# Kernel optimization log

Hardware: AMD Instinct MI355X
Metric: run time of the kernel (lower is better)

The kernel has to match this reference:

```python
import jax, jax.numpy as jnp
import numpy as np

B, NQ, NKV, D, H, HD = 8, 1024, 2048, 1024, 16, 64  # inner_dim = H*HD = 1024


def setup_inputs() -> dict:
    key = jax.random.key(0)
    ks = jax.random.split(key, 10)
    s = 0.02
    return {
        "latent": jax.random.normal(ks[0], (B, NQ, D), jnp.float32),
        "data": jax.random.normal(ks[1], (B, NKV, D), jnp.float32),
        "wq": jax.random.normal(ks[2], (D, H * HD), jnp.float32) * s,
        "bq": jax.random.normal(ks[3], (H * HD,), jnp.float32) * s,
        "wk": jax.random.normal(ks[4], (D, H * HD), jnp.float32) * s,
        "bk": jax.random.normal(ks[5], (H * HD,), jnp.float32) * s,
        "wv": jax.random.normal(ks[6], (D, H * HD), jnp.float32) * s,
        "bv": jax.random.normal(ks[7], (H * HD,), jnp.float32) * s,
        "wo": jax.random.normal(ks[8], (H * HD, D), jnp.float32) * s,
        "bo": jax.random.normal(ks[9], (D,), jnp.float32) * s,
    }


def reference(latent, data, wq, bq, wk, bk, wv, bv, wo, bo):
    scale = HD ** -0.5
    # projections: [b, n, H*HD] -> [b, h, n, d]
    def split_heads(t):
        b, n, _ = t.shape
        return t.reshape(b, n, H, HD).transpose(0, 2, 1, 3)

    q = split_heads(latent @ wq + bq)   # [b, h, nq, d]
    k = split_heads(data @ wk + bk)     # [b, h, nkv, d]
    v = split_heads(data @ wv + bv)     # [b, h, nkv, d]

    scores = jnp.einsum("bhid,bhjd->bhij", q, k) * scale  # [b, h, nq, nkv]
    att = jax.nn.softmax(scores, axis=-1)                  # dropout p=0 (eval)
    out = jnp.einsum("bhij,bhjd->bhid", att, v)            # [b, h, nq, d]
    out = out.transpose(0, 2, 1, 3).reshape(B, NQ, H * HD)
    return out @ wo + bo
```

## Files before the change

### kernel.cpp

```cpp
#include <hip/hip_runtime.h>
#include <hip/hip_bf16.h>
#include <math.h>


using short8  = __attribute__((ext_vector_type(8))) short;
using f32x4   = __attribute__((ext_vector_type(4))) float;
using uint4v  = __attribute__((ext_vector_type(4))) unsigned int;

__device__ __forceinline__ ushort f2bf(float f) {
    unsigned u = __builtin_bit_cast(unsigned, f);
    u = (u + 0x7FFFu + ((u >> 16) & 1u)) >> 16;
    return (ushort)u;
}
__device__ __forceinline__ unsigned pack_bf2(float lo, float hi) {
    unsigned ulo = __builtin_bit_cast(unsigned, lo) + 0x8000u;
    unsigned uhi = __builtin_bit_cast(unsigned, hi) + 0x8000u;
    return __builtin_amdgcn_perm(uhi, ulo, 0x07060302);
}

__device__ __forceinline__ void gld_lds16(const ushort* g, ushort* l) {
    __builtin_amdgcn_global_load_lds(
        (const __attribute__((address_space(1))) unsigned int*)(const void*)g,
        (__attribute__((address_space(3))) unsigned int*)(void*)l,
        16, 0, 0);
}

__global__ void prep_fused(const float* __restrict__ latent, const float* __restrict__ data,
                           const float* __restrict__ wq, const float* __restrict__ wk,
                           const float* __restrict__ wv, const float* __restrict__ wo,
                           ushort* __restrict__ latB, ushort* __restrict__ datB,
                           ushort* __restrict__ wqT, ushort* __restrict__ wkT,
                           ushort* __restrict__ wvT, ushort* __restrict__ woT) {
    __shared__ ushort tile[32][33];
    const int bx  = blockIdx.x;
    const int tid = threadIdx.x;
    if (bx < 12288) {
        const float* in = (bx < 4096) ? latent : data;
        ushort* out     = (bx < 4096) ? latB : datB;
        int idx = (bx < 4096) ? bx : bx - 4096;
        int i = (idx * 256 + tid) * 8;
        float4 a = *(const float4*)(in + i);
        float4 b = *(const float4*)(in + i + 4);
        short8 o;
        o[0] = (short)f2bf(a.x); o[1] = (short)f2bf(a.y);
        o[2] = (short)f2bf(a.z); o[3] = (short)f2bf(a.w);
        o[4] = (short)f2bf(b.x); o[5] = (short)f2bf(b.y);
        o[6] = (short)f2bf(b.z); o[7] = (short)f2bf(b.w);
        *(short8*)(out + i) = o;
        return;
    }
    int rem = bx - 12288;
    int z   = rem >> 10;
    int bxx = rem & 31;
    int byy = (rem >> 5) & 31;
    const float* in = (z == 0) ? wq : (z == 1) ? wk : (z == 2) ? wv : wo;
    ushort* out     = (z == 0) ? wqT : (z == 1) ? wkT : (z == 2) ? wvT : woT;
    int tx = tid & 31, ty = tid >> 5;
    int x = bxx * 32 + tx;
    int y = byy * 32;
#pragma unroll
    for (int i = 0; i < 32; i += 8)
        tile[ty + i][tx] = f2bf(in[(size_t)(y + ty + i) * 1024 + x]);
    __syncthreads();
    int x2 = byy * 32 + tx;
    int y2 = bxx * 32;
#pragma unroll
    for (int i = 0; i < 32; i += 8)
        out[(size_t)(y2 + ty + i) * 1024 + x2] = tile[tx][ty + i];
}

template <int S>
__device__ __forceinline__ void stage_half(const ushort* __restrict__ G, int rbase,
                                           ushort* tile, int H, int kcol,
                                           int wave, int lane) {
#pragma unroll
    for (int c = 0; c < 2; ++c) {
        int rho = c * 64 + wave * 8;
        int gr0 = (rho / S) * (2 * S) + H * S + (rho % S);
        int rig = lane >> 3;
        int q   = (lane & 7) ^ rig;
        gld_lds16(G + (size_t)(rbase + gr0 + rig) * 1024 + kcol + q * 8,
                  tile + gr0 * 64);
    }
}

__device__ __forceinline__ void gemm256_body(
        const ushort* __restrict__ A, const ushort* __restrict__ Bt,
        const float* __restrict__ bias, void* __restrict__ Cv,
        float scale, int mode, int bm, int bn) {
    __shared__ __align__(16) ushort sm[65536];
    ushort* As0 = sm;
    ushort* Bs0 = sm + 16384;
    ushort* As1 = sm + 32768;
    ushort* Bs1 = sm + 49152;

    const int tid  = threadIdx.x;
    const int wave = tid >> 6, lane = tid & 63;
    const int l15 = lane & 15, quad = lane >> 4;
    const int wm = wave >> 2, wn = wave & 3;
    const int m0 = bm * 256, n0 = bn * 256;

    const int rA  = wm * 128 + l15;
    const int rB  = wn * 64 + l15;
    const int cq0 = quad ^ (l15 & 7);
    const int cq1 = (4 + quad) ^ (l15 & 7);

    stage_half<64>(A,  m0, As0, 0, 0,  wave, lane);
    stage_half<32>(Bt, n0, Bs0, 0, 0,  wave, lane);
    stage_half<32>(Bt, n0, Bs0, 1, 0,  wave, lane);
    stage_half<64>(A,  m0, As0, 1, 0,  wave, lane);
    stage_half<64>(A,  m0, As1, 0, 64, wave, lane);
    stage_half<32>(Bt, n0, Bs1, 1, 64, wave, lane);
    stage_half<64>(A,  m0, As1, 1, 64, wave, lane);
    asm volatile("s_waitcnt vmcnt(6)" ::: "memory");
    __builtin_amdgcn_s_barrier();

    f32x4 acc[8][4] = {};

#define LDA(MH)                                                                   \
    _Pragma("unroll")                                                             \
    for (int mi = 0; mi < 4; ++mi) {                                              \
        a[mi][0] = *(const short8*)(Ac + (rA + (MH) * 64 + mi * 16) * 64 + cq0 * 8); \
        a[mi][1] = *(const short8*)(Ac + (rA + (MH) * 64 + mi * 16) * 64 + cq1 * 8); \
    }
#define LDB_ALL                                                                   \
    _Pragma("unroll")                                                             \
    for (int nj = 0; nj < 4; ++nj) {                                              \
        b[nj][0] = *(const short8*)(Bc + (rB + nj * 16) * 64 + cq0 * 8);          \
        b[nj][1] = *(const short8*)(Bc + (rB + nj * 16) * 64 + cq1 * 8);          \
    }
#define MFMA_PHASE(MB, NB)                                                        \
    __builtin_amdgcn_s_barrier();                                                 \
    asm volatile("s_waitcnt lgkmcnt(0)" ::: "memory");                            \
    __builtin_amdgcn_sched_barrier(0);                                            \
    __builtin_amdgcn_s_setprio(1);                                                \
    _Pragma("unroll")                                                             \
    for (int mi = 0; mi < 4; ++mi)                                                \
        _Pragma("unroll")                                                         \
        for (int ni = 0; ni < 2; ++ni)                                            \
            _Pragma("unroll")                                                     \
            for (int kk = 0; kk < 2; ++kk)                                        \
                acc[(MB) * 4 + mi][(NB) * 2 + ni] =                               \
                    __builtin_amdgcn_mfma_f32_16x16x32_bf16(                      \
                        a[mi][kk], b[(NB) * 2 + ni][kk],                          \
                        acc[(MB) * 4 + mi][(NB) * 2 + ni], 0, 0, 0);              \
    __builtin_amdgcn_s_setprio(0);                                                \
    __builtin_amdgcn_s_barrier();

#pragma unroll 2
    for (int g = 0; g < 16; ++g) {
        ushort* Ac = (g & 1) ? As1 : As0;
        ushort* Bc = (g & 1) ? Bs1 : Bs0;
        ushort* Bn = (g & 1) ? Bs0 : Bs1;
        const int k1 = ((g + 1) & 15) * 64;
        const int k2 = ((g + 2) & 15) * 64;
        short8 a[4][2], b[4][2];

        LDA(0) LDB_ALL
        stage_half<32>(Bt, n0, Bn, 0, k1, wave, lane);
        MFMA_PHASE(0, 0)

        stage_half<64>(A, m0, Ac, 0, k2, wave, lane);
        MFMA_PHASE(0, 1)

        LDA(1)
        stage_half<32>(Bt, n0, Bc, 1, k2, wave, lane);
        MFMA_PHASE(1, 1)

        stage_half<64>(A, m0, Ac, 1, k2, wave, lane);
        asm volatile("s_waitcnt vmcnt(6)" ::: "memory");
        MFMA_PHASE(1, 0)
    }
#undef LDA
#undef LDB_ALL
#undef MFMA_PHASE

    asm volatile("s_waitcnt vmcnt(0)" ::: "memory");

    float bvv[4];
    int   cols[4];
#pragma unroll
    for (int n4 = 0; n4 < 4; ++n4) {
        cols[n4] = n0 + wn * 64 + n4 * 16 + l15;
        bvv[n4]  = bias[cols[n4]];
    }
#pragma unroll
    for (int m8 = 0; m8 < 8; ++m8) {
        int rbase = m0 + wm * 128 + m8 * 16 + quad * 4;
#pragma unroll
        for (int n4 = 0; n4 < 4; ++n4) {
            float v[4];
#pragma unroll
            for (int rr = 0; rr < 4; ++rr)
                v[rr] = (acc[m8][n4][rr] + bvv[n4]) * scale;
            if (mode == 1) {
                int kvl = rbase & 2047;
                int pos = (kvl & ~31) + ((kvl >> 2) & 3) * 8 + ((kvl >> 4) & 1) * 4;
                size_t base = ((size_t)((rbase >> 11) * 1024 + cols[n4])) * 2048 + pos;
                uint2 o;
                o.x = pack_bf2(v[0], v[1]);
                o.y = pack_bf2(v[2], v[3]);
                *(uint2*)((ushort*)Cv + base) = o;
            } else if (mode == 0) {
#pragma unroll
                for (int rr = 0; rr < 4; ++rr)
                    ((ushort*)Cv)[(size_t)(rbase + rr) * 1024 + cols[n4]] = f2bf(v[rr]);
            } else {
#pragma unroll
                for (int rr = 0; rr < 4; ++rr)
                    ((float*)Cv)[(size_t)(rbase + rr) * 1024 + cols[n4]] = v[rr];
            }
        }
    }
}

__global__ __launch_bounds__(512, 2) void proj_qkv(
        const ushort* __restrict__ latB, const ushort* __restrict__ datB,
        const ushort* __restrict__ wqT, const ushort* __restrict__ wkT,
        const ushort* __restrict__ wvT,
        const float* __restrict__ bq, const float* __restrict__ bk,
        const float* __restrict__ bv,
        ushort* __restrict__ Qb, ushort* __restrict__ Kb, ushort* __restrict__ Vtb,
        float qscale) {
    int bid = ((int)blockIdx.x & 7) * 80 + ((int)blockIdx.x >> 3);
    const ushort* A;
    const ushort* W;
    const float*  bias;
    void*         C;
    float sc;
    int mode, idx;
    if (bid < 128)      { A = latB; W = wqT; bias = bq; C = Qb;  sc = qscale; mode = 0; idx = bid; }
    else if (bid < 384) { A = datB; W = wkT; bias = bk; C = Kb;  sc = 1.f;    mode = 0; idx = bid - 128; }
    else                { A = datB; W = wvT; bias = bv; C = Vtb; sc = 1.f;    mode = 1; idx = bid - 384; }
    gemm256_body(A, W, bias, C, sc, mode, idx >> 2, idx & 3);
}

template <int MODE>
__global__ void gemm_bt(const ushort* __restrict__ A, const ushort* __restrict__ Bt,
                        const float* __restrict__ bias, void* __restrict__ Cv,
                        int K, float scale) {
    __shared__ __align__(16) ushort As[128 * 32];
    __shared__ __align__(16) ushort Bs[128 * 32];
    const int tid  = threadIdx.x;
    const int wave = tid >> 6, lane = tid & 63;
    const int l15 = lane & 15, quad = lane >> 4;
    const int wm = wave & 1, wn = wave >> 1;
    const int m0 = blockIdx.x * 128;
    const int n0 = blockIdx.y * 128;

    f32x4 acc[4][4] = {};

    for (int k0 = 0; k0 < K; k0 += 32) {
        __syncthreads();
#pragma unroll
        for (int i = 0; i < 2; ++i) {
            int f   = (i * 256 + tid) * 8;
            int row = f >> 5, col = f & 31;
            gld_lds16(A  + (size_t)(m0 + row) * K + k0 + col, As + (i * 256 + wave * 64) * 8);
            gld_lds16(Bt + (size_t)(n0 + row) * K + k0 + col, Bs + (i * 256 + wave * 64) * 8);
        }
        __syncthreads();

        short8 a[4], b[4];
#pragma unroll
        for (int mi = 0; mi < 4; ++mi)
            a[mi] = *(const short8*)(As + (wm * 64 + mi * 16 + l15) * 32 + quad * 8);
#pragma unroll
        for (int ni = 0; ni < 4; ++ni)
            b[ni] = *(const short8*)(Bs + (wn * 64 + ni * 16 + l15) * 32 + quad * 8);
#pragma unroll
        for (int mi = 0; mi < 4; ++mi)
#pragma unroll
            for (int ni = 0; ni < 4; ++ni)
                acc[mi][ni] = __builtin_amdgcn_mfma_f32_16x16x32_bf16(a[mi], b[ni], acc[mi][ni], 0, 0, 0);
    }

    float bv[4];
    int   cols[4];
#pragma unroll
    for (int ni = 0; ni < 4; ++ni) {
        cols[ni] = n0 + wn * 64 + ni * 16 + l15;
        bv[ni]   = bias[cols[ni]];
    }
#pragma unroll
    for (int mi = 0; mi < 4; ++mi) {
        int rbase = m0 + wm * 64 + mi * 16 + quad * 4;
#pragma unroll
        for (int ni = 0; ni < 4; ++ni) {
            float v[4];
#pragma unroll
            for (int rr = 0; rr < 4; ++rr)
                v[rr] = (acc[mi][ni][rr] + bv[ni]) * scale;
            if (MODE == 1) {
                int kvl = rbase & 2047;
                int pos = (kvl & ~31) + ((kvl >> 2) & 3) * 8 + ((kvl >> 4) & 1) * 4;
                size_t base = ((size_t)((rbase >> 11) * 1024 + cols[ni])) * 2048 + pos;
                uint2 o;
                o.x = pack_bf2(v[0], v[1]);
                o.y = pack_bf2(v[2], v[3]);
                *(uint2*)((ushort*)Cv + base) = o;
            } else {
#pragma unroll
                for (int rr = 0; rr < 4; ++rr) {
                    int row = rbase + rr;
                    if (MODE == 0)
                        ((ushort*)Cv)[(size_t)row * 1024 + cols[ni]] = f2bf(v[rr]);
                    else
                        ((float*)Cv)[(size_t)row * 1024 + cols[ni]] = v[rr];
                }
            }
        }
    }
}

__global__ __launch_bounds__(256, 4) void attn_fused(const ushort* __restrict__ Q,
                                                     const ushort* __restrict__ K,
                                                     const ushort* __restrict__ Vt,
                                                     ushort* __restrict__ O) {
    __shared__ __align__(16) ushort smem[2 * 8192];
    ushort* Ks  = smem;
    ushort* Vts = smem + 8192;

    const int tid  = threadIdx.x;
    const int wave = tid >> 6, lane = tid & 63;
    const int l15 = lane & 15, quad = lane >> 4;
    const int bx = blockIdx.x;
    const int bh = bx & 127, h = bh & 15, b = bh >> 4;
    const int q0 = (bx >> 7) * 128;

    const ushort* Qg = Q + ((size_t)(b * 1024 + q0)) * 1024 + h * 64;
    const ushort* Kg = K + ((size_t)(b * 2048)) * 1024 + h * 64;
    const ushort* Vg = Vt + ((size_t)(b * 1024 + h * 64)) * 2048;

    short8 bq[2][2];
#pragma unroll
    for (int qt = 0; qt < 2; ++qt) {
        int row = wave * 32 + qt * 16 + l15;
#pragma unroll
        for (int ks = 0; ks < 2; ++ks)
            bq[ks][qt] = *(const short8*)(Qg + (size_t)row * 1024 + ks * 32 + quad * 8);
    }

    f32x4 Oacc[4][2] = {};
    float l_run[2] = {0.f, 0.f};

    const int rig = lane >> 3;
    const int scb8 = (lane & 7) ^ rig;
    const int riv = lane >> 4;
    const int cb16 = lane & 15;

    for (int kv0 = 0; kv0 < 2048; kv0 += 128) {
        __syncthreads();
#pragma unroll
        for (int g = 0; g < 4; ++g) {
            int G = wave * 4 + g;
            gld_lds16(Kg + (size_t)(kv0 + G * 8 + rig) * 1024 + scb8 * 8, Ks + G * 512);
            int vrow = G * 4 + riv;
            int scv = cb16 ^ (vrow & 15);
            gld_lds16(Vg + (size_t)vrow * 2048 + kv0 + scv * 8, Vts + G * 512);
        }
        __syncthreads();

        __builtin_amdgcn_s_setprio(1);
        unsigned pk[8][2][2];
#pragma unroll
        for (int kvt = 0; kvt < 8; ++kvt) {
            f32x4 s0 = {}, s1 = {};
#pragma unroll
            for (int ks = 0; ks < 2; ++ks) {
                int ck = ((ks * 4 + quad) ^ (l15 & 7)) * 8;
                short8 ak = *(const short8*)(Ks + (kvt * 16 + l15) * 64 + ck);
                s0 = __builtin_amdgcn_mfma_f32_16x16x32_bf16(ak, bq[ks][0], s0, 0, 0, 0);
                s1 = __builtin_amdgcn_mfma_f32_16x16x32_bf16(ak, bq[ks][1], s1, 0, 0, 0);
            }
            float p0[4], p1[4];
#pragma unroll
            for (int rr = 0; rr < 4; ++rr) {
                p0[rr] = __builtin_amdgcn_exp2f(s0[rr]);
                p1[rr] = __builtin_amdgcn_exp2f(s1[rr]);
                l_run[0] += p0[rr];
                l_run[1] += p1[rr];
            }
            pk[kvt][0][0] = pack_bf2(p0[0], p0[1]);
            pk[kvt][0][1] = pack_bf2(p0[2], p0[3]);
            pk[kvt][1][0] = pack_bf2(p1[0], p1[1]);
            pk[kvt][1][1] = pack_bf2(p1[2], p1[3]);
        }

#pragma unroll
        for (int sp = 0; sp < 4; ++sp) {
#pragma unroll
            for (int dt = 0; dt < 4; ++dt) {
                int cv = ((sp * 4 + quad) ^ l15) * 8;
                short8 av = *(const short8*)(Vts + (dt * 16 + l15) * 128 + cv);
#pragma unroll
                for (int qt = 0; qt < 2; ++qt) {
                    uint4v u = {pk[2 * sp][qt][0], pk[2 * sp][qt][1],
                                pk[2 * sp + 1][qt][0], pk[2 * sp + 1][qt][1]};
                    short8 bp = __builtin_bit_cast(short8, u);
                    Oacc[dt][qt] = __builtin_amdgcn_mfma_f32_16x16x32_bf16(av, bp, Oacc[dt][qt], 0, 0, 0);
                }
            }
        }
        __builtin_amdgcn_s_setprio(0);
    }

#pragma unroll
    for (int qt = 0; qt < 2; ++qt) {
        float l = l_run[qt];
        l += __shfl_xor(l, 16);
        l += __shfl_xor(l, 32);
        float inv = 1.f / l;
        int qg = q0 + wave * 32 + qt * 16 + l15;
#pragma unroll
        for (int dt = 0; dt < 4; ++dt) {
            uint2 o;
            o.x = pack_bf2(Oacc[dt][qt][0] * inv, Oacc[dt][qt][1] * inv);
            o.y = pack_bf2(Oacc[dt][qt][2] * inv, Oacc[dt][qt][3] * inv);
            *(uint2*)(O + ((size_t)(b * 1024 + qg)) * 1024 + h * 64 + dt * 16 + quad * 4) = o;
        }
    }
}

extern "C" void kernel_launch(void* const* d_in, const int* in_sizes, int n_in,
                              void* d_out, int out_size, void* d_ws, size_t ws_size,
                              hipStream_t stream) {
    const float* latent = (const float*)d_in[0];
    const float* data   = (const float*)d_in[1];
    const float* wq     = (const float*)d_in[2];
    const float* bq     = (const float*)d_in[3];
    const float* wk     = (const float*)d_in[4];
    const float* bk     = (const float*)d_in[5];
    const float* wv     = (const float*)d_in[6];
    const float* bv     = (const float*)d_in[7];
    const float* wo     = (const float*)d_in[8];
    const float* bo     = (const float*)d_in[9];
    float* out = (float*)d_out;

    ushort* ws   = (ushort*)d_ws;
    ushort* wqT  = ws;
    ushort* wkT  = wqT + (1u << 20);
    ushort* wvT  = wkT + (1u << 20);
    ushort* woT  = wvT + (1u << 20);
    ushort* latB = woT + (1u << 20);
    ushort* datB = latB + (8u << 20);
    ushort* Qb   = datB + (16u << 20);
    ushort* Kb   = Qb + (8u << 20);
    ushort* Vtb  = Kb + (16u << 20);
    ushort* AO   = latB;

    prep_fused<<<dim3(16384), 256, 0, stream>>>(latent, data, wq, wk, wv, wo,
                                                latB, datB, wqT, wkT, wvT, woT);

    const float qscale = 0.125f * 1.44269504088896340736f;
    proj_qkv<<<dim3(640), 512, 0, stream>>>(latB, datB, wqT, wkT, wvT,
                                            bq, bk, bv, Qb, Kb, Vtb, qscale);
    attn_fused<<<dim3(1024), 256, 0, stream>>>(Qb, Kb, Vtb, AO);
    gemm_bt<2><<<dim3(64, 8), 256, 0, stream>>>(AO, woT, bo, out, 1024, 1.0f);
}
```

Baseline: 364.5 us.

## Split trailing V-projection tiles into 128-row half tiles to balance the QKV grid

The fused QKV projection previously launched 640 blocks, each computing a 256x256 tile. That leaves a partial second wave when two blocks fit per CU. Now the first 512 blocks keep the 256x256 path, covering Q, K and half of V. The remaining 128 V tiles are computed as 256 blocks of 128x256 by a new gemm128_body with its own staging helper and a transposed-V epilogue. This is meant to shrink the wave-quantization tail, at the cost of lower per-block reuse on the half tiles and more kernel code.

```diff
diff --git a/kernel.cpp b/kernel.cpp
--- a/kernel.cpp
+++ b/kernel.cpp
@@ -83,12 +83,20 @@
                   tile + gr0 * 64);
     }
 }
+__device__ __forceinline__ void stage_a128(const ushort* __restrict__ G, int rbase,
+                                           ushort* tile, int H, int kcol,
+                                           int wave, int lane) {
+    int gr0 = H * 64 + wave * 8;
+    int rig = lane >> 3;
+    int q   = (lane & 7) ^ rig;
+    gld_lds16(G + (size_t)(rbase + gr0 + rig) * 1024 + kcol + q * 8,
+              tile + gr0 * 64);
+}
 
 __device__ __forceinline__ void gemm256_body(
         const ushort* __restrict__ A, const ushort* __restrict__ Bt,
         const float* __restrict__ bias, void* __restrict__ Cv,
-        float scale, int mode, int bm, int bn) {
-    __shared__ __align__(16) ushort sm[65536];
+        ushort* sm, float scale, int mode, int bm, int bn) {
     ushort* As0 = sm;
     ushort* Bs0 = sm + 16384;
     ushort* As1 = sm + 32768;
@@ -214,6 +222,114 @@
     }
 }
 
+__device__ __forceinline__ void gemm128_body(
+        const ushort* __restrict__ A, const ushort* __restrict__ Bt,
+        const float* __restrict__ bias, ushort* __restrict__ Cv,
+        ushort* sm, int m0, int n0) {
+    ushort* As0 = sm;
+    ushort* Bs0 = sm + 8192;
+    ushort* As1 = sm + 24576;
+    ushort* Bs1 = sm + 32768;
+
+    const int tid  = threadIdx.x;
+    const int wave = tid >> 6, lane = tid & 63;
+    const int l15 = lane & 15, quad = lane >> 4;
+    const int wm = wave >> 2, wn = wave & 3;
+
+    const int rA  = wm * 64 + l15;
+    const int rB  = wn * 64 + l15;
+    const int cq0 = quad ^ (l15 & 7);
+    const int cq1 = (4 + quad) ^ (l15 & 7);
+
+    stage_a128(A, m0, As0, 0, 0, wave, lane);
+    stage_half<32>(Bt, n0, Bs0, 0, 0, wave, lane);
+    stage_half<32>(Bt, n0, Bs0, 1, 0, wave, lane);
+    stage_a128(A, m0, As0, 1, 0, wave, lane);
+    stage_a128(A, m0, As1, 0, 64, wave, lane);
+    stage_half<32>(Bt, n0, Bs1, 1, 64, wave, lane);
+    stage_a128(A, m0, As1, 1, 64, wave, lane);
+    asm volatile("s_waitcnt vmcnt(4)" ::: "memory");
+    __builtin_amdgcn_s_barrier();
+
+    f32x4 acc[4][4] = {};
+
+#define MFMA_PHASE_N(NI)                                                          \
+    __builtin_amdgcn_s_barrier();                                                 \
+    asm volatile("s_waitcnt lgkmcnt(0)" ::: "memory");                            \
+    __builtin_amdgcn_sched_barrier(0);                                            \
+    __builtin_amdgcn_s_setprio(1);                                                \
+    _Pragma("unroll")                                                             \
+    for (int mi = 0; mi < 4; ++mi)                                                \
+        _Pragma("unroll")                                                         \
+        for (int kk = 0; kk < 2; ++kk)                                            \
+            acc[mi][NI] = __builtin_amdgcn_mfma_f32_16x16x32_bf16(                \
+                a[mi][kk], b[NI][kk], acc[mi][NI], 0, 0, 0);                      \
+    __builtin_amdgcn_s_setprio(0);                                                \
+    __builtin_amdgcn_s_barrier();
+
+#pragma unroll 2
+    for (int g = 0; g < 16; ++g) {
+        ushort* Ac = (g & 1) ? As1 : As0;
+        ushort* Bc = (g & 1) ? Bs1 : Bs0;
+        ushort* Bn = (g & 1) ? Bs0 : Bs1;
+        const int k1 = ((g + 1) & 15) * 64;
+        const int k2 = ((g + 2) & 15) * 64;
+        short8 a[4][2], b[4][2];
+
+#pragma unroll
+        for (int mi = 0; mi < 4; ++mi) {
+            a[mi][0] = *(const short8*)(Ac + (rA + mi * 16) * 64 + cq0 * 8);
+            a[mi][1] = *(const short8*)(Ac + (rA + mi * 16) * 64 + cq1 * 8);
+        }
+#pragma unroll
+        for (int nj = 0; nj < 4; ++nj) {
+            b[nj][0] = *(const short8*)(Bc + (rB + nj * 16) * 64 + cq0 * 8);
+            b[nj][1] = *(const short8*)(Bc + (rB + nj * 16) * 64 + cq1 * 8);
+        }
+        stage_half<32>(Bt, n0, Bn, 0, k1, wave, lane);
+        MFMA_PHASE_N(0)
+
+        stage_a128(A, m0, Ac, 0, k2, wave, lane);
+        MFMA_PHASE_N(1)
+
+        stage_half<32>(Bt, n0, Bc, 1, k2, wave, lane);
+        MFMA_PHASE_N(2)
+
+        stage_a128(A, m0, Ac, 1, k2, wave, lane);
+        asm volatile("s_waitcnt vmcnt(4)" ::: "memory");
+        MFMA_PHASE_N(3)
+    }
+#undef MFMA_PHASE_N
+
+    asm volatile("s_waitcnt vmcnt(0)" ::: "memory");
+
+    float bvv[4];
+    int   cols[4];
+#pragma unroll
+    for (int n4 = 0; n4 < 4; ++n4) {
+        cols[n4] = n0 + wn * 64 + n4 * 16 + l15;
+        bvv[n4]  = bias[cols[n4]];
+    }
+#pragma unroll
+    for (int m4 = 0; m4 < 4; ++m4) {
+        int rbase = m0 + wm * 64 + m4 * 16 + quad * 4;
+#pragma unroll
+        for (int n4 = 0; n4 < 4; ++n4) {
+            float v[4];
+#pragma unroll
+            for (int rr = 0; rr < 4; ++rr)
+                v[rr] = acc[m4][n4][rr] + bvv[n4];
+            int kvl = rbase & 2047;
+            int pos = (kvl & ~31) + ((kvl >> 2) & 3) * 8 + ((kvl >> 4) & 1) * 4;
+            size_t base = ((size_t)((rbase >> 11) * 1024 + cols[n4])) * 2048 + pos;
+            uint2 o;
+            o.x = pack_bf2(v[0], v[1]);
+            o.y = pack_bf2(v[2], v[3]);
+            *(uint2*)(Cv + base) = o;
+        }
+    }
+}
+
 __global__ __launch_bounds__(512, 2) void proj_qkv(
         const ushort* __restrict__ latB, const ushort* __restrict__ datB,
         const ushort* __restrict__ wqT, const ushort* __restrict__ wkT,
@@ -222,17 +338,25 @@
         const float* __restrict__ bv,
         ushort* __restrict__ Qb, ushort* __restrict__ Kb, ushort* __restrict__ Vtb,
         float qscale) {
-    int bid = ((int)blockIdx.x & 7) * 80 + ((int)blockIdx.x >> 3);
-    const ushort* A;
-    const ushort* W;
-    const float*  bias;
-    void*         C;
-    float sc;
-    int mode, idx;
-    if (bid < 128)      { A = latB; W = wqT; bias = bq; C = Qb;  sc = qscale; mode = 0; idx = bid; }
-    else if (bid < 384) { A = datB; W = wkT; bias = bk; C = Kb;  sc = 1.f;    mode = 0; idx = bid - 128; }
-    else                { A = datB; W = wvT; bias = bv; C = Vtb; sc = 1.f;    mode = 1; idx = bid - 384; }
-    gemm256_body(A, W, bias, C, sc, mode, idx >> 2, idx & 3);
+    __shared__ __align__(16) ushort sm[65536];
+    int bx = blockIdx.x;
+    if (bx < 512) {
+        int bid = (bx & 7) * 64 + (bx >> 3);
+        const ushort* A; const ushort* W; const float* bias;
+        void* C; float sc; int mode, idx;
+        if (bid < 128)      { A = latB; W = wqT; bias = bq; C = Qb;  sc = qscale; mode = 0; idx = bid; }
+        else if (bid < 384) { A = datB; W = wkT; bias = bk; C = Kb;  sc = 1.f;    mode = 0; idx = bid - 128; }
+        else                { A = datB; W = wvT; bias = bv; C = Vtb; sc = 1.f;    mode = 1; idx = bid - 384; }
+        gemm256_body(A, W, bias, C, sm, sc, mode, idx >> 2, idx & 3);
+    } else {
+        int t  = bx - 512;
+        int tt = (t & 7) * 32 + (t >> 3);
+        int vtile = 128 + (tt >> 1);
+        int mhalf = tt & 1;
+        int m0 = (vtile >> 2) * 256 + mhalf * 128;
+        int n0 = (vtile & 3) * 256;
+        gemm128_body(datB, wvT, bv, Vtb, sm, m0, n0);
+    }
 }
 
 template <int MODE>
@@ -453,7 +577,7 @@
                                                 latB, datB, wqT, wkT, wvT, woT);
 
     const float qscale = 0.125f * 1.44269504088896340736f;
-    proj_qkv<<<dim3(640), 512, 0, stream>>>(latB, datB, wqT, wkT, wvT,
+    proj_qkv<<<dim3(768), 512, 0, stream>>>(latB, datB, wqT, wkT, wvT,
                                             bq, bk, bv, Qb, Kb, Vtb, qscale);
     attn_fused<<<dim3(1024), 256, 0, stream>>>(Qb, Kb, Vtb, AO);
     gemm_bt<2><<<dim3(64, 8), 256, 0, stream>>>(AO, woT, bo, out, 1024, 1.0f);
```

Result: faster. 354.5 us (-2.7%).
